# Optimization experiments

Measured on AMD Instinct MI355X. Metric: run time of the kernel, lower is better.

The kernel has to match this reference:

```python
import jax, jax.numpy as jnp
import numpy as np

B, T, D = 1, 4096, 2048
H, HKV = 16, 4
DH = D // H            # 128
GROUP = H // HKV       # 4
ROPE_BASE = 10000.0


def setup_inputs() -> dict:
    key = jax.random.key(0)
    kx, kq, kk, kv, ko = jax.random.split(key, 5)
    s = 0.02
    return {
        "x": jax.random.normal(kx, (B, T, D), dtype=jnp.float32),
        "Wq": jax.random.normal(kq, (D, D), dtype=jnp.float32) * s,
        "Wk": jax.random.normal(kk, (D, HKV * DH), dtype=jnp.float32) * s,
        "Wv": jax.random.normal(kv, (D, HKV * DH), dtype=jnp.float32) * s,
        "Wo": jax.random.normal(ko, (D, D), dtype=jnp.float32) * s,
    }


def _rope_sincos(t, half):
    inv_freq = 1.0 / (ROPE_BASE ** (jnp.arange(half, dtype=jnp.float32) / half))
    ang = jnp.arange(t, dtype=jnp.float32)[:, None] * inv_freq  # [T, half]
    # broadcast over batch and head dims: [1, T, 1, half]
    return jnp.sin(ang)[None, :, None, :], jnp.cos(ang)[None, :, None, :]


def _apply_rope(x, sin, cos, half):
    x1, x2 = x[..., :half], x[..., half:]
    return jnp.concatenate([x1 * cos - x2 * sin, x1 * sin + x2 * cos], axis=-1)


def reference(x, Wq, Wk, Wv, Wo):
    b, t, d = x.shape
    q = (x @ Wq).reshape(b, t, H, DH)      # [B,T,H,Dh], H ordered (Hkv, group)
    k = (x @ Wk).reshape(b, t, HKV, DH)    # [B,T,Hkv,Dh]
    v = (x @ Wv).reshape(b, t, HKV, DH)

    half = DH // 2
    sin, cos = _rope_sincos(t, half)
    q = _apply_rope(q, sin, cos, half)
    k = _apply_rope(k, sin, cos, half)

    # GQA without materializing repeated K/V: split q heads into (kv_head, group)
    qg = q.reshape(b, t, HKV, GROUP, DH)
    att = jnp.einsum('bthgd,bshd->bhgts', qg, k) / np.float32(np.sqrt(DH))
    causal = jnp.tril(jnp.ones((t, t), dtype=bool))
    att = jnp.where(causal[None, None, None, :, :], att, -jnp.inf)
    att = jax.nn.softmax(att, axis=-1)
    y = jnp.einsum('bhgts,bshd->bthgd', att, v).reshape(b, t, d)
    return y @ Wo
```

## Files before the change

kernel.cpp:

```cpp
#include <hip/hip_runtime.h>
#include <hip/hip_bf16.h>

#define TT 4096
#define DD 2048
#define NH 16
#define NKV 4
#define DHD 128
#define NQKV 3072

typedef __attribute__((ext_vector_type(8))) short short8;
typedef __attribute__((ext_vector_type(4))) float f32x4;
typedef __hip_bfloat16 bf16;

#define GLOAD_LDS16(g, l)                                                \
    __builtin_amdgcn_global_load_lds(                                    \
        (const __attribute__((address_space(1))) unsigned int*)(g),      \
        (__attribute__((address_space(3))) unsigned int*)(l), 16, 0, 0)

__global__ void cast_x_kernel(const float* __restrict__ x, bf16* __restrict__ xb, int n) {
    int i = (blockIdx.x * blockDim.x + threadIdx.x) * 4;
    if (i >= n) return;
    float4 v = *(const float4*)(x + i);
    xb[i + 0] = __float2bfloat16(v.x);
    xb[i + 1] = __float2bfloat16(v.y);
    xb[i + 2] = __float2bfloat16(v.z);
    xb[i + 3] = __float2bfloat16(v.w);
}

__global__ void transpose_cast_all(const float* __restrict__ Wq, const float* __restrict__ Wk,
                                   const float* __restrict__ Wv, const float* __restrict__ Wo,
                                   bf16* __restrict__ Wt, bf16* __restrict__ Wot) {
    __shared__ float tile[32][33];
    const float* in;
    bf16* out;
    int N, rowOff;
    switch (blockIdx.z) {
        case 0: in = Wq; out = Wt; N = 2048; rowOff = 0; break;
        case 1: in = Wk; out = Wt; N = 512; rowOff = 2048; break;
        case 2: in = Wv; out = Wt; N = 512; rowOff = 2560; break;
        default: in = Wo; out = Wot; N = 2048; rowOff = 0; break;
    }
    int n0 = blockIdx.y * 32;
    if (n0 >= N) return;
    int k0 = blockIdx.x * 32;
    int tx = threadIdx.x, ty = threadIdx.y;
#pragma unroll
    for (int i = 0; i < 4; ++i)
        tile[ty + i * 8][tx] = in[(size_t)(k0 + ty + i * 8) * N + n0 + tx];
    __syncthreads();
#pragma unroll
    for (int i = 0; i < 4; ++i)
        out[(size_t)(rowOff + n0 + ty + i * 8) * 2048 + k0 + tx] = __float2bfloat16(tile[tx][ty + i * 8]);
}

template <bool OUT_BF16>
__global__ __launch_bounds__(256) void gemm_bt_kernel(const bf16* __restrict__ A,
                                                      const bf16* __restrict__ Bt,
                                                      void* __restrict__ C,
                                                      int M, int N, int K) {
    __shared__ bf16 As[128 * 32];
    __shared__ bf16 Bs[128 * 32];
    int bn0 = blockIdx.x * 128, bm0 = blockIdx.y * 128;
    int tid = threadIdx.x;
    int wave = tid >> 6, lane = tid & 63, quad = lane >> 4, l15 = lane & 15;
    int wm = (wave >> 1) * 64, wn = (wave & 1) * 64;

    int srow = wave * 32 + (lane >> 2);
    int scol = (lane & 3) * 8;
    const bf16* gA = A + (size_t)(bm0 + srow) * K + scol;
    const bf16* gB = Bt + (size_t)(bn0 + srow) * K + scol;
    bf16* lA = As + srow * 32 + scol;
    bf16* lB = Bs + srow * 32 + scol;

    f32x4 zero = {0.f, 0.f, 0.f, 0.f};
    f32x4 acc[4][4];
#pragma unroll
    for (int i = 0; i < 4; ++i)
#pragma unroll
        for (int j = 0; j < 4; ++j) acc[i][j] = zero;

    for (int k0 = 0; k0 < K; k0 += 32) {
        GLOAD_LDS16(gA + k0, lA);
        GLOAD_LDS16(gA + k0 + (size_t)16 * K, lA + 16 * 32);
        GLOAD_LDS16(gB + k0, lB);
        GLOAD_LDS16(gB + k0 + (size_t)16 * K, lB + 16 * 32);
        __syncthreads();
        short8 af[4], bfr[4];
#pragma unroll
        for (int i = 0; i < 4; ++i) af[i] = *(const short8*)&As[(wm + i * 16 + l15) * 32 + quad * 8];
#pragma unroll
        for (int j = 0; j < 4; ++j) bfr[j] = *(const short8*)&Bs[(wn + j * 16 + l15) * 32 + quad * 8];
#pragma unroll
        for (int i = 0; i < 4; ++i)
#pragma unroll
            for (int j = 0; j < 4; ++j)
                acc[i][j] = __builtin_amdgcn_mfma_f32_16x16x32_bf16(af[i], bfr[j], acc[i][j], 0, 0, 0);
        __syncthreads();
    }
#pragma unroll
    for (int i = 0; i < 4; ++i)
#pragma unroll
        for (int j = 0; j < 4; ++j)
#pragma unroll
            for (int r = 0; r < 4; ++r) {
                int row = bm0 + wm + i * 16 + quad * 4 + r;
                int col = bn0 + wn + j * 16 + l15;
                float v = acc[i][j][r];
                if (OUT_BF16)
                    ((bf16*)C)[(size_t)row * N + col] = __float2bfloat16(v);
                else
                    ((float*)C)[(size_t)row * N + col] = v;
            }
}

__global__ void rope_split_kernel(const bf16* __restrict__ QKV, bf16* __restrict__ Qs,
                                  bf16* __restrict__ Ks, bf16* __restrict__ Vt) {
    int slot = blockIdx.x * 4 + (threadIdx.x >> 6);
    int d = threadIdx.x & 63;
    int t = slot / 24, c = slot % 24;
    const bf16* base = QKV + (size_t)t * NQKV;
    int off = (c < 16) ? c * 128 : (c < 20) ? 2048 + (c - 16) * 128 : 2560 + (c - 20) * 128;
    float x1 = __bfloat162float(base[off + d]);
    float x2 = __bfloat162float(base[off + 64 + d]);
    float o1, o2;
    if (c < 20) {
        float invf = __expf((float)d * -0.14391156831f);
        float ang = (float)t * invf;
        float sn = sinf(ang), cs = cosf(ang);
        o1 = x1 * cs - x2 * sn;
        o2 = x1 * sn + x2 * cs;
    } else {
        o1 = x1;
        o2 = x2;
    }
    if (c < 16) {
        const float scale = 0.12751741f;
        o1 *= scale;
        o2 *= scale;
        bf16* dst = Qs + ((size_t)c * TT + t) * DHD;
        dst[d] = __float2bfloat16(o1);
        dst[d + 64] = __float2bfloat16(o2);
    } else if (c < 20) {
        bf16* dst = Ks + ((size_t)(c - 16) * TT + t) * DHD;
        dst[d] = __float2bfloat16(o1);
        dst[d + 64] = __float2bfloat16(o2);
    } else {
        int gg = c - 20;
        Vt[((size_t)gg * DHD + d) * TT + t] = __float2bfloat16(o1);
        Vt[((size_t)gg * DHD + d + 64) * TT + t] = __float2bfloat16(o2);
    }
}

__global__ __launch_bounds__(256, 4) void attn_kernel(const bf16* __restrict__ Qs,
                                                      const bf16* __restrict__ Ks,
                                                      const bf16* __restrict__ Vt,
                                                      bf16* __restrict__ Y) {
    __shared__ bf16 KsL[64 * 128];
    __shared__ bf16 VtL[128 * 64];
    __shared__ bf16 PsL[4][16 * 64];
    int h = blockIdx.y, bpair = blockIdx.x, g = h >> 2;
    int tid = threadIdx.x, wave = tid >> 6, lane = tid & 63, quad = lane >> 4, l15 = lane & 15;

    const bf16* kg = Ks + (size_t)g * TT * DHD;
    const bf16* vg = Vt + (size_t)g * DHD * TT;
    f32x4 zero = {0.f, 0.f, 0.f, 0.f};

    for (int pass = 0; pass < 2; ++pass) {
        int qt = (pass == 0) ? bpair : 63 - bpair;
        int qbase = qt * 64 + wave * 16;

        short8 qf[4];
        const bf16* qptr = Qs + ((size_t)h * TT + qbase + l15) * DHD + quad * 8;
#pragma unroll
        for (int ks = 0; ks < 4; ++ks) qf[ks] = *(const short8*)(qptr + ks * 32);

        f32x4 acc[8];
#pragma unroll
        for (int i = 0; i < 8; ++i) acc[i] = zero;
        float m_i = -1e30f, l_i = 0.f;

        for (int kt = 0; kt <= qt; ++kt) {
            int kb = kt * 64;
            bool diag = (kt == qt);
            short8 kv[4], vv[4];
            int krow[4], kc[4], vrow[4], vc[4];
#pragma unroll
            for (int r = 0; r < 4; ++r) {
                int idx = r * 256 + tid;
                krow[r] = idx >> 4;
                kc[r] = idx & 15;
                kv[r] = *(const short8*)(kg + (size_t)(kb + krow[r]) * DHD + kc[r] * 8);
                vrow[r] = idx >> 3;
                vc[r] = idx & 7;
                vv[r] = *(const short8*)(vg + (size_t)vrow[r] * TT + kb + vc[r] * 8);
            }
            __syncthreads();
#pragma unroll
            for (int r = 0; r < 4; ++r) {
                *(short8*)&KsL[krow[r] * 128 + ((kc[r] ^ (krow[r] & 15)) * 8)] = kv[r];
                *(short8*)&VtL[vrow[r] * 64 + ((vc[r] ^ (vrow[r] & 7)) * 8)] = vv[r];
            }
            __syncthreads();

            f32x4 s[4];
#pragma unroll
            for (int nt = 0; nt < 4; ++nt) {
                if (!diag || nt <= wave) {
                    s[nt] = zero;
#pragma unroll
                    for (int ks = 0; ks < 4; ++ks) {
                        int ch = (ks * 4 + quad) ^ l15;
                        short8 kf = *(const short8*)&KsL[(nt * 16 + l15) * 128 + ch * 8];
                        s[nt] = __builtin_amdgcn_mfma_f32_16x16x32_bf16(kf, qf[ks], s[nt], 0, 0, 0);
                    }
                    if (diag && nt == wave) {
#pragma unroll
                        for (int r = 0; r < 4; ++r)
                            if (quad * 4 + r > l15) s[nt][r] = -1e30f;
                    }
                } else {
#pragma unroll
                    for (int r = 0; r < 4; ++r) s[nt][r] = -1e30f;
                }
            }

            float mloc = -1e30f;
#pragma unroll
            for (int nt = 0; nt < 4; ++nt)
#pragma unroll
                for (int r = 0; r < 4; ++r) mloc = fmaxf(mloc, s[nt][r]);
            mloc = fmaxf(mloc, __shfl_xor(mloc, 16));
            mloc = fmaxf(mloc, __shfl_xor(mloc, 32));
            float mnew = fmaxf(m_i, mloc);
            float alpha = exp2f(m_i - mnew);
            m_i = mnew;
            float sl = 0.f;
#pragma unroll
            for (int nt = 0; nt < 4; ++nt)
#pragma unroll
                for (int r = 0; r < 4; ++r) {
                    s[nt][r] = exp2f(s[nt][r] - mnew);
                    sl += s[nt][r];
                }
            sl += __shfl_xor(sl, 16);
            sl += __shfl_xor(sl, 32);
            l_i = l_i * alpha + sl;
#pragma unroll
            for (int d8 = 0; d8 < 8; ++d8)
#pragma unroll
                for (int r = 0; r < 4; ++r) acc[d8][r] *= alpha;

#pragma unroll
            for (int nt = 0; nt < 4; ++nt)
#pragma unroll
                for (int rr = 0; rr < 2; ++rr) {
                    int col = nt * 16 + quad * 4 + rr * 2;
                    int ch = (col >> 3) ^ (l15 & 7);
                    __hip_bfloat162 pk;
                    pk.x = __float2bfloat16(s[nt][rr * 2]);
                    pk.y = __float2bfloat16(s[nt][rr * 2 + 1]);
                    *(__hip_bfloat162*)&PsL[wave][l15 * 64 + ch * 8 + (col & 7)] = pk;
                }
            asm volatile("s_waitcnt lgkmcnt(0)" ::: "memory");

            int kkmax = diag ? (wave >> 1) + 1 : 2;
#pragma unroll
            for (int kk = 0; kk < 2; ++kk) {
                if (kk < kkmax) {
                    int chp = (kk * 4 + quad) ^ (l15 & 7);
                    short8 pf = *(const short8*)&PsL[wave][l15 * 64 + chp * 8];
#pragma unroll
                    for (int d8 = 0; d8 < 8; ++d8) {
                        short8 vf = *(const short8*)&VtL[(d8 * 16 + l15) * 64 + chp * 8];
                        acc[d8] = __builtin_amdgcn_mfma_f32_16x16x32_bf16(vf, pf, acc[d8], 0, 0, 0);
                    }
                }
            }
        }

        float linv = 1.0f / l_i;
        __syncthreads();
        bf16* ow = KsL + wave * 2048;
#pragma unroll
        for (int d8 = 0; d8 < 8; ++d8)
#pragma unroll
            for (int rr = 0; rr < 2; ++rr) {
                int colD = d8 * 16 + quad * 4 + rr * 2;
                int ch = (colD >> 3) ^ (l15 & 7);
                __hip_bfloat162 o2;
                o2.x = __float2bfloat16(acc[d8][rr * 2] * linv);
                o2.y = __float2bfloat16(acc[d8][rr * 2 + 1] * linv);
                *(__hip_bfloat162*)&ow[l15 * 128 + ch * 8 + (colD & 7)] = o2;
            }
        asm volatile("s_waitcnt lgkmcnt(0)" ::: "memory");
#pragma unroll
        for (int c = 0; c < 4; ++c) {
            int chunk = quad * 4 + c;
            int ch = chunk ^ (l15 & 7);
            short8 ov = *(const short8*)&ow[l15 * 128 + ch * 8];
            *(short8*)&Y[(size_t)(qbase + l15) * DD + h * DHD + chunk * 8] = ov;
        }
        __syncthreads();
    }
}

extern "C" void kernel_launch(void* const* d_in, const int* in_sizes, int n_in,
                              void* d_out, int out_size, void* d_ws, size_t ws_size,
                              hipStream_t stream) {
    const float* x = (const float*)d_in[0];
    const float* Wq = (const float*)d_in[1];
    const float* Wk = (const float*)d_in[2];
    const float* Wv = (const float*)d_in[3];
    const float* Wo = (const float*)d_in[4];

    char* ws = (char*)d_ws;
    size_t off = 0;
    auto alloc = [&](size_t bytes) {
        void* p = ws + off;
        off += (bytes + 255) & ~(size_t)255;
        return p;
    };
    bf16* xb = (bf16*)alloc((size_t)TT * DD * 2);
    bf16* Wt = (bf16*)alloc((size_t)NQKV * DD * 2);
    bf16* Wot = (bf16*)alloc((size_t)DD * DD * 2);
    bf16* QKVb = (bf16*)alloc((size_t)TT * NQKV * 2);
    bf16* Qs = (bf16*)alloc((size_t)NH * TT * DHD * 2);
    bf16* Ksb = (bf16*)alloc((size_t)NKV * TT * DHD * 2);
    bf16* Vtb = (bf16*)alloc((size_t)NKV * DHD * TT * 2);
    bf16* Yb = (bf16*)alloc((size_t)TT * DD * 2);

    cast_x_kernel<<<(TT * DD / 4 + 255) / 256, 256, 0, stream>>>(x, xb, TT * DD);
    transpose_cast_all<<<dim3(64, 64, 4), dim3(32, 8), 0, stream>>>(Wq, Wk, Wv, Wo, Wt, Wot);

    gemm_bt_kernel<true><<<dim3(NQKV / 128, TT / 128), 256, 0, stream>>>(xb, Wt, QKVb, TT, NQKV, DD);
    rope_split_kernel<<<TT * 24 / 4, 256, 0, stream>>>(QKVb, Qs, Ksb, Vtb);
    attn_kernel<<<dim3(32, NH), 256, 0, stream>>>(Qs, Ksb, Vtb, Yb);
    gemm_bt_kernel<false><<<dim3(DD / 128, TT / 128), 256, 0, stream>>>(Yb, Wot, d_out, TT, DD, DD);
}
```

Before: 418.8 us.

## Split attention KV loop across two wave groups and merge softmax partials

Doubles the attention block to 512 threads, with two groups of four waves each processing alternating KV tiles for the same query tile. The two online-softmax partial states are merged through shared memory at the end of each pass. The rescale of the accumulator is skipped when no running max increased. This aims to double per-block parallelism on a grid of only 512 blocks, at the cost of 80KB of LDS per block, which limits occupancy, plus an extra merge step with several block-wide barriers.

```diff
diff --git a/kernel.cpp b/kernel.cpp
--- a/kernel.cpp
+++ b/kernel.cpp
@@ -151,15 +151,22 @@
     }
 }
 
-__global__ __launch_bounds__(256, 4) void attn_kernel(const bf16* __restrict__ Qs,
+__global__ __launch_bounds__(512, 4) void attn_kernel(const bf16* __restrict__ Qs,
                                                       const bf16* __restrict__ Ks,
                                                       const bf16* __restrict__ Vt,
                                                       bf16* __restrict__ Y) {
-    __shared__ bf16 KsL[64 * 128];
-    __shared__ bf16 VtL[128 * 64];
-    __shared__ bf16 PsL[4][16 * 64];
+    __shared__ char smem[81920];
     int h = blockIdx.y, bpair = blockIdx.x, g = h >> 2;
     int tid = threadIdx.x, wave = tid >> 6, lane = tid & 63, quad = lane >> 4, l15 = lane & 15;
+    int grp = wave >> 2;
+    int w = wave & 3;
+    int gtid = tid & 255;
+
+    bf16* KsL = (bf16*)(smem + grp * 32768);
+    bf16* VtL = (bf16*)(smem + grp * 32768 + 16384);
+    bf16* PsW = (bf16*)(smem + 65536) + wave * (16 * 64);
+    float* Obuf = (float*)(smem + 32768);
+    float* mlbuf = (float*)(smem + 80896);
 
     const bf16* kg = Ks + (size_t)g * TT * DHD;
     const bf16* vg = Vt + (size_t)g * DHD * TT;
@@ -167,7 +174,7 @@
 
     for (int pass = 0; pass < 2; ++pass) {
         int qt = (pass == 0) ? bpair : 63 - bpair;
-        int qbase = qt * 64 + wave * 16;
+        int qbase = qt * 64 + w * 16;
 
         short8 qf[4];
         const bf16* qptr = Qs + ((size_t)h * TT + qbase + l15) * DHD + quad * 8;
@@ -179,126 +186,170 @@
         for (int i = 0; i < 8; ++i) acc[i] = zero;
         float m_i = -1e30f, l_i = 0.f;
 
-        for (int kt = 0; kt <= qt; ++kt) {
+        int nIter = (qt >> 1) + 1;
+        for (int it = 0; it < nIter; ++it) {
+            int kt = it * 2 + grp;
+            bool active = (kt <= qt);
+            bool diag = (kt == qt);
             int kb = kt * 64;
-            bool diag = (kt == qt);
             short8 kv[4], vv[4];
             int krow[4], kc[4], vrow[4], vc[4];
-#pragma unroll
-            for (int r = 0; r < 4; ++r) {
-                int idx = r * 256 + tid;
-                krow[r] = idx >> 4;
-                kc[r] = idx & 15;
-                kv[r] = *(const short8*)(kg + (size_t)(kb + krow[r]) * DHD + kc[r] * 8);
-                vrow[r] = idx >> 3;
-                vc[r] = idx & 7;
-                vv[r] = *(const short8*)(vg + (size_t)vrow[r] * TT + kb + vc[r] * 8);
+            if (active) {
+#pragma unroll
+                for (int r = 0; r < 4; ++r) {
+                    int idx = r * 256 + gtid;
+                    krow[r] = idx >> 4;
+                    kc[r] = idx & 15;
+                    kv[r] = *(const short8*)(kg + (size_t)(kb + krow[r]) * DHD + kc[r] * 8);
+                    vrow[r] = idx >> 3;
+                    vc[r] = idx & 7;
+                    vv[r] = *(const short8*)(vg + (size_t)vrow[r] * TT + kb + vc[r] * 8);
+                }
             }
             __syncthreads();
-#pragma unroll
-            for (int r = 0; r < 4; ++r) {
-                *(short8*)&KsL[krow[r] * 128 + ((kc[r] ^ (krow[r] & 15)) * 8)] = kv[r];
-                *(short8*)&VtL[vrow[r] * 64 + ((vc[r] ^ (vrow[r] & 7)) * 8)] = vv[r];
+            if (active) {
+#pragma unroll
+                for (int r = 0; r < 4; ++r) {
+                    *(short8*)&KsL[krow[r] * 128 + ((kc[r] ^ (krow[r] & 15)) * 8)] = kv[r];
+                    *(short8*)&VtL[vrow[r] * 64 + ((vc[r] ^ (vrow[r] & 7)) * 8)] = vv[r];
+                }
             }
             __syncthreads();
 
-            f32x4 s[4];
-#pragma unroll
-            for (int nt = 0; nt < 4; ++nt) {
-                if (!diag || nt <= wave) {
-                    s[nt] = zero;
-#pragma unroll
-                    for (int ks = 0; ks < 4; ++ks) {
-                        int ch = (ks * 4 + quad) ^ l15;
-                        short8 kf = *(const short8*)&KsL[(nt * 16 + l15) * 128 + ch * 8];
-                        s[nt] = __builtin_amdgcn_mfma_f32_16x16x32_bf16(kf, qf[ks], s[nt], 0, 0, 0);
+            if (active) {
+                f32x4 s[4];
+#pragma unroll
+                for (int nt = 0; nt < 4; ++nt) {
+                    if (!diag || nt <= w) {
+                        s[nt] = zero;
+#pragma unroll
+                        for (int ks = 0; ks < 4; ++ks) {
+                            int ch = (ks * 4 + quad) ^ l15;
+                            short8 kf = *(const short8*)&KsL[(nt * 16 + l15) * 128 + ch * 8];
+                            s[nt] = __builtin_amdgcn_mfma_f32_16x16x32_bf16(kf, qf[ks], s[nt], 0, 0, 0);
+                        }
+                        if (diag && nt == w) {
+#pragma unroll
+                            for (int r = 0; r < 4; ++r)
+                                if (quad * 4 + r > l15) s[nt][r] = -1e30f;
+                        }
+                    } else {
+#pragma unroll
+                        for (int r = 0; r < 4; ++r) s[nt][r] = -1e30f;
                     }
-                    if (diag && nt == wave) {
-#pragma unroll
-                        for (int r = 0; r < 4; ++r)
-                            if (quad * 4 + r > l15) s[nt][r] = -1e30f;
+                }
+
+                float mloc = -1e30f;
+#pragma unroll
+                for (int nt = 0; nt < 4; ++nt)
+#pragma unroll
+                    for (int r = 0; r < 4; ++r) mloc = fmaxf(mloc, s[nt][r]);
+                mloc = fmaxf(mloc, __shfl_xor(mloc, 16));
+                mloc = fmaxf(mloc, __shfl_xor(mloc, 32));
+                float mnew = fmaxf(m_i, mloc);
+                bool up = __any(mloc > m_i);
+                float alpha = up ? exp2f(m_i - mnew) : 1.0f;
+                float sl = 0.f;
+#pragma unroll
+                for (int nt = 0; nt < 4; ++nt)
+#pragma unroll
+                    for (int r = 0; r < 4; ++r) {
+                        s[nt][r] = exp2f(s[nt][r] - mnew);
+                        sl += s[nt][r];
                     }
-                } else {
-#pragma unroll
-                    for (int r = 0; r < 4; ++r) s[nt][r] = -1e30f;
-                }
-            }
-
-            float mloc = -1e30f;
-#pragma unroll
-            for (int nt = 0; nt < 4; ++nt)
-#pragma unroll
-                for (int r = 0; r < 4; ++r) mloc = fmaxf(mloc, s[nt][r]);
-            mloc = fmaxf(mloc, __shfl_xor(mloc, 16));
-            mloc = fmaxf(mloc, __shfl_xor(mloc, 32));
-            float mnew = fmaxf(m_i, mloc);
-            float alpha = exp2f(m_i - mnew);
-            m_i = mnew;
-            float sl = 0.f;
-#pragma unroll
-            for (int nt = 0; nt < 4; ++nt)
-#pragma unroll
-                for (int r = 0; r < 4; ++r) {
-                    s[nt][r] = exp2f(s[nt][r] - mnew);
-                    sl += s[nt][r];
-                }
-            sl += __shfl_xor(sl, 16);
-            sl += __shfl_xor(sl, 32);
-            l_i = l_i * alpha + sl;
+                sl += __shfl_xor(sl, 16);
+                sl += __shfl_xor(sl, 32);
+                l_i = l_i * alpha + sl;
+                m_i = mnew;
+                if (up) {
+#pragma unroll
+                    for (int d8 = 0; d8 < 8; ++d8)
+#pragma unroll
+                        for (int r = 0; r < 4; ++r) acc[d8][r] *= alpha;
+                }
+
+#pragma unroll
+                for (int nt = 0; nt < 4; ++nt)
+#pragma unroll
+                    for (int rr = 0; rr < 2; ++rr) {
+                        int col = nt * 16 + quad * 4 + rr * 2;
+                        int ch = (col >> 3) ^ (l15 & 7);
+                        __hip_bfloat162 pk;
+                        pk.x = __float2bfloat16(s[nt][rr * 2]);
+                        pk.y = __float2bfloat16(s[nt][rr * 2 + 1]);
+                        *(__hip_bfloat162*)&PsW[l15 * 64 + ch * 8 + (col & 7)] = pk;
+                    }
+                asm volatile("s_waitcnt lgkmcnt(0)" ::: "memory");
+
+                int kkmax = diag ? (w >> 1) + 1 : 2;
+#pragma unroll
+                for (int kk = 0; kk < 2; ++kk) {
+                    if (kk < kkmax) {
+                        int chp = (kk * 4 + quad) ^ (l15 & 7);
+                        short8 pf = *(const short8*)&PsW[l15 * 64 + chp * 8];
+#pragma unroll
+                        for (int d8 = 0; d8 < 8; ++d8) {
+                            short8 vf = *(const short8*)&VtL[(d8 * 16 + l15) * 64 + chp * 8];
+                            acc[d8] = __builtin_amdgcn_mfma_f32_16x16x32_bf16(vf, pf, acc[d8], 0, 0, 0);
+                        }
+                    }
+                }
+            }
+        }
+
+        __syncthreads();
+        if (quad == 0) {
+            mlbuf[(wave * 16 + l15) * 2] = m_i;
+            mlbuf[(wave * 16 + l15) * 2 + 1] = l_i;
+        }
+        __syncthreads();
+        if (grp == 1) {
+            float m_a = mlbuf[(w * 16 + l15) * 2];
+            float mm = fmaxf(m_a, m_i);
+            float fb = exp2f(m_i - mm);
+            float* ob = Obuf + (w * 16 + l15) * 132;
+#pragma unroll
+            for (int d8 = 0; d8 < 8; ++d8) {
+                f32x4 t = acc[d8] * fb;
+                *(f32x4*)&ob[d8 * 16 + quad * 4] = t;
+            }
+        }
+        __syncthreads();
+        if (grp == 0) {
+            float m_b = mlbuf[((w + 4) * 16 + l15) * 2];
+            float l_b = mlbuf[((w + 4) * 16 + l15) * 2 + 1];
+            float mm = fmaxf(m_i, m_b);
+            float fa = exp2f(m_i - mm);
+            float fb = exp2f(m_b - mm);
+            float lt = l_i * fa + l_b * fb;
+            float* ob = Obuf + (w * 16 + l15) * 132;
+#pragma unroll
+            for (int d8 = 0; d8 < 8; ++d8) {
+                f32x4 t = *(const f32x4*)&ob[d8 * 16 + quad * 4];
+                acc[d8] = acc[d8] * fa + t;
+            }
+            float linv = 1.0f / lt;
+
+            bf16* ow = (bf16*)smem + w * 2048;
 #pragma unroll
             for (int d8 = 0; d8 < 8; ++d8)
 #pragma unroll
-                for (int r = 0; r < 4; ++r) acc[d8][r] *= alpha;
-
-#pragma unroll
-            for (int nt = 0; nt < 4; ++nt)
-#pragma unroll
                 for (int rr = 0; rr < 2; ++rr) {
-                    int col = nt * 16 + quad * 4 + rr * 2;
-                    int ch = (col >> 3) ^ (l15 & 7);
-                    __hip_bfloat162 pk;
-                    pk.x = __float2bfloat16(s[nt][rr * 2]);
-                    pk.y = __float2bfloat16(s[nt][rr * 2 + 1]);
-                    *(__hip_bfloat162*)&PsL[wave][l15 * 64 + ch * 8 + (col & 7)] = pk;
+                    int colD = d8 * 16 + quad * 4 + rr * 2;
+                    int ch = (colD >> 3) ^ (l15 & 7);
+                    __hip_bfloat162 o2;
+                    o2.x = __float2bfloat16(acc[d8][rr * 2] * linv);
+                    o2.y = __float2bfloat16(acc[d8][rr * 2 + 1] * linv);
+                    *(__hip_bfloat162*)&ow[l15 * 128 + ch * 8 + (colD & 7)] = o2;
                 }
             asm volatile("s_waitcnt lgkmcnt(0)" ::: "memory");
-
-            int kkmax = diag ? (wave >> 1) + 1 : 2;
-#pragma unroll
-            for (int kk = 0; kk < 2; ++kk) {
-                if (kk < kkmax) {
-                    int chp = (kk * 4 + quad) ^ (l15 & 7);
-                    short8 pf = *(const short8*)&PsL[wave][l15 * 64 + chp * 8];
-#pragma unroll
-                    for (int d8 = 0; d8 < 8; ++d8) {
-                        short8 vf = *(const short8*)&VtL[(d8 * 16 + l15) * 64 + chp * 8];
-                        acc[d8] = __builtin_amdgcn_mfma_f32_16x16x32_bf16(vf, pf, acc[d8], 0, 0, 0);
-                    }
-                }
-            }
-        }
-
-        float linv = 1.0f / l_i;
-        __syncthreads();
-        bf16* ow = KsL + wave * 2048;
-#pragma unroll
-        for (int d8 = 0; d8 < 8; ++d8)
-#pragma unroll
-            for (int rr = 0; rr < 2; ++rr) {
-                int colD = d8 * 16 + quad * 4 + rr * 2;
-                int ch = (colD >> 3) ^ (l15 & 7);
-                __hip_bfloat162 o2;
-                o2.x = __float2bfloat16(acc[d8][rr * 2] * linv);
-                o2.y = __float2bfloat16(acc[d8][rr * 2 + 1] * linv);
-                *(__hip_bfloat162*)&ow[l15 * 128 + ch * 8 + (colD & 7)] = o2;
-            }
-        asm volatile("s_waitcnt lgkmcnt(0)" ::: "memory");
-#pragma unroll
-        for (int c = 0; c < 4; ++c) {
-            int chunk = quad * 4 + c;
-            int ch = chunk ^ (l15 & 7);
-            short8 ov = *(const short8*)&ow[l15 * 128 + ch * 8];
-            *(short8*)&Y[(size_t)(qbase + l15) * DD + h * DHD + chunk * 8] = ov;
+#pragma unroll
+            for (int c = 0; c < 4; ++c) {
+                int chunk = quad * 4 + c;
+                int ch = chunk ^ (l15 & 7);
+                short8 ov = *(const short8*)&ow[l15 * 128 + ch * 8];
+                *(short8*)&Y[(size_t)(qbase + l15) * DD + h * DHD + chunk * 8] = ov;
+            }
         }
         __syncthreads();
     }
@@ -334,6 +385,6 @@
 
     gemm_bt_kernel<true><<<dim3(NQKV / 128, TT / 128), 256, 0, stream>>>(xb, Wt, QKVb, TT, NQKV, DD);
     rope_split_kernel<<<TT * 24 / 4, 256, 0, stream>>>(QKVb, Qs, Ksb, Vtb);
-    attn_kernel<<<dim3(32, NH), 256, 0, stream>>>(Qs, Ksb, Vtb, Yb);
+    attn_kernel<<<dim3(32, NH), 512, 0, stream>>>(Qs, Ksb, Vtb, Yb);
     gemm_bt_kernel<false><<<dim3(DD / 128, TT / 128), 256, 0, stream>>>(Yb, Wot, d_out, TT, DD, DD);
 }
```

After: 516.7 us. 1.23x slower.
